# Performance work log

Hardware: AMD Instinct MI355X
Metric: run time of the kernel (lower is better)

Reference implementation:

```python
import jax, jax.numpy as jnp
import numpy as np

D_MODEL = 1024
NUM_HEAD = 16
D_K = D_MODEL // NUM_HEAD


def setup_inputs() -> dict:
    key = jax.random.key(0)
    ks = jax.random.split(key, 9)
    s = 1.0 / np.sqrt(D_MODEL)
    return {
        "x": jax.random.normal(ks[0], (2, 2048, D_MODEL), dtype=jnp.float32),
        "Wq": jax.random.normal(ks[1], (D_MODEL, D_MODEL), dtype=jnp.float32) * s,
        "bq": jax.random.normal(ks[2], (D_MODEL,), dtype=jnp.float32) * s,
        "Wk": jax.random.normal(ks[3], (D_MODEL, D_MODEL), dtype=jnp.float32) * s,
        "bk": jax.random.normal(ks[4], (D_MODEL,), dtype=jnp.float32) * s,
        "Wv": jax.random.normal(ks[5], (D_MODEL, D_MODEL), dtype=jnp.float32) * s,
        "bv": jax.random.normal(ks[6], (D_MODEL,), dtype=jnp.float32) * s,
        "Wo": jax.random.normal(ks[7], (D_MODEL, D_MODEL), dtype=jnp.float32) * s,
        "bo": jax.random.normal(ks[8], (D_MODEL,), dtype=jnp.float32) * s,
    }


def reference(x, Wq, bq, Wk, bk, Wv, bv, Wo, bo):
    B, S, _ = x.shape
    # QKV projections: [B,S,D] -> [B,H,S,d_k]
    def proj(W, b):
        y = jnp.einsum("bsd,df->bsf", x, W) + b
        return y.reshape(B, S, NUM_HEAD, D_K).transpose(0, 2, 1, 3)

    Q = proj(Wq, bq)
    K = proj(Wk, bk)
    V = proj(Wv, bv)
    scale = 1.0 / jnp.sqrt(jnp.asarray(D_K, dtype=x.dtype))
    attn = jnp.einsum("bhqd,bhkd->bhqk", Q, K) * scale  # [B,H,S,S]
    probs = jax.nn.softmax(attn, axis=-1)
    out = jnp.einsum("bhqk,bhkd->bhqd", probs, V)  # [B,H,S,d_k]
    out = out.transpose(0, 2, 1, 3).reshape(B, S, D_MODEL)
    return jnp.einsum("bsd,df->bsf", out, Wo) + bo
```

## Files before the change

### kernel.cpp

```cpp
#include <hip/hip_runtime.h>
#include <hip/hip_bf16.h>
#include <math.h>

constexpr int DM = 1024;
constexpr int NH = 16;
constexpr int DK = 64;
constexpr int SQ = 2048;
constexpr int BB = 2;
constexpr int MR = BB * SQ;

typedef short bf16x8 __attribute__((ext_vector_type(8)));
typedef float f32x4 __attribute__((ext_vector_type(4)));

__device__ inline unsigned short f2bf(float f) {
  unsigned u = __float_as_uint(f);
  unsigned r = (u + 0x7fffu + ((u >> 16) & 1u)) >> 16;
  return (unsigned short)r;
}

__device__ inline int fswz(int r) { return (r & 7) ^ ((r >> 3) & 7); }
__device__ inline int swz(int r, int c) {
  return r * 64 + ((((c >> 3) ^ fswz(r)) & 7) << 3) + (c & 7);
}

__global__ __launch_bounds__(256)
void cast_kernel(const float* __restrict__ in, unsigned short* __restrict__ out, int n8) {
  int i = blockIdx.x * 256 + threadIdx.x;
  if (i >= n8) return;
  float4 a = *(const float4*)&in[(size_t)i * 8];
  float4 b = *(const float4*)&in[(size_t)i * 8 + 4];
  ushort4 lo = {f2bf(a.x), f2bf(a.y), f2bf(a.z), f2bf(a.w)};
  ushort4 hi = {f2bf(b.x), f2bf(b.y), f2bf(b.z), f2bf(b.w)};
  *(ushort4*)&out[(size_t)i * 8] = lo;
  *(ushort4*)&out[(size_t)i * 8 + 4] = hi;
}

__global__ __launch_bounds__(256)
void transpose_cast_kernel(const float* __restrict__ W, unsigned short* __restrict__ Wt) {
  __shared__ float tl[32][33];
  const int tx = threadIdx.x & 31, ty = threadIdx.x >> 5;
  const int x0 = blockIdx.x * 32, y0 = blockIdx.y * 32;
  #pragma unroll
  for (int i = 0; i < 4; ++i)
    tl[ty + i * 8][tx] = W[(size_t)(y0 + ty + i * 8) * DM + x0 + tx];
  __syncthreads();
  #pragma unroll
  for (int i = 0; i < 4; ++i)
    Wt[(size_t)(x0 + ty + i * 8) * DM + y0 + tx] = f2bf(tl[tx][ty + i * 8]);
}

template<int MODE>
__global__ __launch_bounds__(256)
void mfma_gemm(const unsigned short* __restrict__ A, const unsigned short* __restrict__ Bt,
               const float* __restrict__ bias, void* __restrict__ outp)
{
  constexpr int K = DM, N = DM;
  __shared__ unsigned short As[2][128 * 64];
  __shared__ unsigned short Bs[2][128 * 64];
  const int t = threadIdx.x;
  const int w = t >> 6, ln = t & 63;
  const int wr = w >> 1, wc = w & 1;
  const int rb = blockIdx.y * 128, cb = blockIdx.x * 128;

  f32x4 acc[4][4] = {};

  auto stage = [&](int buf, int k0) {
    #pragma unroll
    for (int j = 0; j < 4; ++j) {
      const int rows8 = (w * 4 + j) * 8;
      const int r = rows8 + (ln >> 3);
      const int gc = (((ln & 7) ^ fswz(r)) & 7) * 8;
      __builtin_amdgcn_global_load_lds(
          (const __attribute__((address_space(1))) void*)&A[(size_t)(rb + r) * K + k0 + gc],
          (__attribute__((address_space(3))) void*)&As[buf][rows8 * 64], 16, 0, 0);
      __builtin_amdgcn_global_load_lds(
          (const __attribute__((address_space(1))) void*)&Bt[(size_t)(cb + r) * K + k0 + gc],
          (__attribute__((address_space(3))) void*)&Bs[buf][rows8 * 64], 16, 0, 0);
    }
  };

  stage(0, 0);
  asm volatile("s_waitcnt vmcnt(0)" ::: "memory");
  __builtin_amdgcn_s_barrier();

  for (int it = 0; it < K / 64; ++it) {
    const int buf = it & 1;
    if (it < K / 64 - 1) stage(buf ^ 1, (it + 1) * 64);
    const int rsel = ln & 15;
    #pragma unroll
    for (int kk = 0; kk < 2; ++kk) {
      const int ko = kk * 32 + (ln >> 4) * 8;
      bf16x8 af[4], bfr[4];
      #pragma unroll
      for (int m = 0; m < 4; ++m)
        af[m] = *(const bf16x8*)&As[buf][swz(wr * 64 + m * 16 + rsel, ko)];
      #pragma unroll
      for (int n = 0; n < 4; ++n)
        bfr[n] = *(const bf16x8*)&Bs[buf][swz(wc * 64 + n * 16 + rsel, ko)];
      #pragma unroll
      for (int m = 0; m < 4; ++m)
        #pragma unroll
        for (int n = 0; n < 4; ++n)
          acc[m][n] = __builtin_amdgcn_mfma_f32_16x16x32_bf16(af[m], bfr[n], acc[m][n], 0, 0, 0);
    }
    asm volatile("s_waitcnt vmcnt(0)" ::: "memory");
    __builtin_amdgcn_s_barrier();
  }

  const int cl = ln & 15, rg = (ln >> 4) * 4;
  #pragma unroll
  for (int m = 0; m < 4; ++m) {
    #pragma unroll
    for (int i = 0; i < 4; ++i) {
      const int r = rb + wr * 64 + m * 16 + rg + i;
      #pragma unroll
      for (int n = 0; n < 4; ++n) {
        const int c = cb + wc * 64 + n * 16 + cl;
        float v = acc[m][n][i] + bias[c];
        if (MODE == 3) v *= 0.125f;
        if (MODE == 0) {
          ((float*)outp)[(size_t)r * N + c] = v;
        } else {
          const int b = r >> 11, s = r & 2047;
          const int h = c >> 6, d = c & 63;
          ((unsigned short*)outp)[(((size_t)(b * NH + h)) * SQ + s) * DK + d] = f2bf(v);
        }
      }
    }
  }
}

__global__ __launch_bounds__(512, 4)
void attn_mfma(const unsigned short* __restrict__ Qp, const unsigned short* __restrict__ Kp,
               const unsigned short* __restrict__ Vp, unsigned short* __restrict__ ctx)
{
  __shared__ unsigned short Qs[128 * 64];
  __shared__ unsigned short Ks[64 * 64];
  __shared__ unsigned short Vt[64 * 64];
  __shared__ unsigned short Pl[8 * 16 * 64];
  const int t = threadIdx.x, w = t >> 6, ln = t & 63;
  const int bh = blockIdx.y, q0 = blockIdx.x * 128;
  const unsigned short* Qb = Qp + (size_t)bh * SQ * DK;
  const unsigned short* Kb = Kp + (size_t)bh * SQ * DK;
  const unsigned short* Vb = Vp + (size_t)bh * SQ * DK;

  #pragma unroll
  for (int i = 0; i < 2; ++i) {
    int g = t + i * 512, r = g >> 3, cg = g & 7;
    uint4 qv = *(const uint4*)&Qb[(size_t)(q0 + r) * DK + cg * 8];
    *(uint4*)&Qs[r * 64 + (((cg ^ fswz(r)) & 7) << 3)] = qv;
  }
  __syncthreads();
  const int rsel = ln & 15, ko = (ln >> 4) * 8;
  bf16x8 qf[2];
  #pragma unroll
  for (int kw = 0; kw < 2; ++kw)
    qf[kw] = *(const bf16x8*)&Qs[swz(w * 16 + rsel, ko + 32 * kw)];

  f32x4 acc2[4] = {};
  float m = -1e30f, l = 0.f;

  const int r0 = t >> 3, cg0 = t & 7;
  uint4 kg = *(const uint4*)&Kb[(size_t)r0 * DK + cg0 * 8];
  uint4 vg = *(const uint4*)&Vb[(size_t)r0 * DK + cg0 * 8];

  for (int c0 = 0; c0 < SQ; c0 += 64) {
    __syncthreads();
    *(uint4*)&Ks[r0 * 64 + (((cg0 ^ fswz(r0)) & 7) << 3)] = kg;
    {
      const unsigned short* vv = (const unsigned short*)&vg;
      const int d0 = cg0 * 8;
      #pragma unroll
      for (int e = 0; e < 8; ++e)
        Vt[swz(d0 + e, r0)] = vv[e];
    }
    __syncthreads();

    if (c0 + 64 < SQ) {
      kg = *(const uint4*)&Kb[(size_t)(c0 + 64 + r0) * DK + cg0 * 8];
      vg = *(const uint4*)&Vb[(size_t)(c0 + 64 + r0) * DK + cg0 * 8];
    }

    f32x4 s[4] = {};
    #pragma unroll
    for (int kw = 0; kw < 2; ++kw)
      #pragma unroll
      for (int fr = 0; fr < 4; ++fr) {
        bf16x8 kf = *(const bf16x8*)&Ks[swz(fr * 16 + rsel, ko + 32 * kw)];
        s[fr] = __builtin_amdgcn_mfma_f32_16x16x32_bf16(kf, qf[kw], s[fr], 0, 0, 0);
      }

    float t0 = fmaxf(fmaxf(s[0][0], s[0][1]), fmaxf(s[0][2], s[0][3]));
    float t1 = fmaxf(fmaxf(s[1][0], s[1][1]), fmaxf(s[1][2], s[1][3]));
    float t2 = fmaxf(fmaxf(s[2][0], s[2][1]), fmaxf(s[2][2], s[2][3]));
    float t3 = fmaxf(fmaxf(s[3][0], s[3][1]), fmaxf(s[3][2], s[3][3]));
    float tm = fmaxf(fmaxf(t0, t1), fmaxf(t2, t3));
    tm = fmaxf(tm, __shfl_xor(tm, 16));
    tm = fmaxf(tm, __shfl_xor(tm, 32));

    if (__any((tm - m) > 8.f)) {
      const float mnew = fmaxf(m, tm);
      const float corr = __expf(m - mnew);
      float ci[4];
      #pragma unroll
      for (int i = 0; i < 4; ++i) ci[i] = __shfl(corr, (ln >> 4) * 4 + i);
      #pragma unroll
      for (int n = 0; n < 4; ++n)
        #pragma unroll
        for (int i = 0; i < 4; ++i) acc2[n][i] *= ci[i];
      l *= corr;
      m = mnew;
    }

    float p[4][4];
    #pragma unroll
    for (int fr = 0; fr < 4; ++fr)
      #pragma unroll
      for (int i = 0; i < 4; ++i)
        p[fr][i] = __expf(s[fr][i] - m);
    float a0 = (p[0][0] + p[0][1]) + (p[0][2] + p[0][3]);
    float a1 = (p[1][0] + p[1][1]) + (p[1][2] + p[1][3]);
    float a2 = (p[2][0] + p[2][1]) + (p[2][2] + p[2][3]);
    float a3 = (p[3][0] + p[3][1]) + (p[3][2] + p[3][3]);
    float ps = (a0 + a1) + (a2 + a3);
    ps += __shfl_xor(ps, 16);
    ps += __shfl_xor(ps, 32);
    l += ps;

    #pragma unroll
    for (int fr = 0; fr < 4; ++fr) {
      unsigned r01, r23;
      asm("v_cvt_pk_bf16_f32 %0, %1, %2" : "=v"(r01) : "v"(p[fr][0]), "v"(p[fr][1]));
      asm("v_cvt_pk_bf16_f32 %0, %1, %2" : "=v"(r23) : "v"(p[fr][2]), "v"(p[fr][3]));
      uint2 pv = {r01, r23};
      const int kk0 = (ln >> 4) * 4 + fr * 16;
      *(uint2*)&Pl[w * 1024 + swz(rsel, kk0)] = pv;
    }

    #pragma unroll
    for (int kw = 0; kw < 2; ++kw) {
      bf16x8 pf = *(const bf16x8*)&Pl[w * 1024 + swz(rsel, ko + 32 * kw)];
      #pragma unroll
      for (int n = 0; n < 4; ++n) {
        bf16x8 vf = *(const bf16x8*)&Vt[swz(n * 16 + rsel, ko + 32 * kw)];
        acc2[n] = __builtin_amdgcn_mfma_f32_16x16x32_bf16(pf, vf, acc2[n], 0, 0, 0);
      }
    }
  }

  const float rl = 1.0f / l;
  float ri[4];
  #pragma unroll
  for (int i = 0; i < 4; ++i) ri[i] = __shfl(rl, (ln >> 4) * 4 + i);
  const int b = bh >> 4, h = bh & 15;
  #pragma unroll
  for (int n = 0; n < 4; ++n)
    #pragma unroll
    for (int i = 0; i < 4; ++i) {
      const int srow = q0 + w * 16 + (ln >> 4) * 4 + i;
      ctx[((size_t)(b * SQ + srow)) * DM + h * 64 + n * 16 + rsel] =
          f2bf(acc2[n][i] * ri[i]);
    }
}

extern "C" void kernel_launch(void* const* d_in, const int* in_sizes, int n_in,
                              void* d_out, int out_size, void* d_ws, size_t ws_size,
                              hipStream_t stream) {
  const float* x  = (const float*)d_in[0];
  const float* Wq = (const float*)d_in[1];
  const float* bq = (const float*)d_in[2];
  const float* Wk = (const float*)d_in[3];
  const float* bk = (const float*)d_in[4];
  const float* Wv = (const float*)d_in[5];
  const float* bv = (const float*)d_in[6];
  const float* Wo = (const float*)d_in[7];
  const float* bo = (const float*)d_in[8];
  float* out = (float*)d_out;

  unsigned short* xb   = (unsigned short*)d_ws;
  unsigned short* Wtq  = xb  + (size_t)MR * DM;
  unsigned short* Wtk  = Wtq + (size_t)DM * DM;
  unsigned short* Wtv  = Wtk + (size_t)DM * DM;
  unsigned short* Wto  = Wtv + (size_t)DM * DM;
  unsigned short* Qb   = Wto + (size_t)DM * DM;
  unsigned short* Kb   = Qb  + (size_t)MR * DM;
  unsigned short* Vb   = Kb  + (size_t)MR * DM;
  unsigned short* ctxb = Vb  + (size_t)MR * DM;

  cast_kernel<<<(MR * DM / 8 + 255) / 256, 256, 0, stream>>>(x, xb, MR * DM / 8);
  dim3 tg(DM / 32, DM / 32);
  transpose_cast_kernel<<<tg, 256, 0, stream>>>(Wq, Wtq);
  transpose_cast_kernel<<<tg, 256, 0, stream>>>(Wk, Wtk);
  transpose_cast_kernel<<<tg, 256, 0, stream>>>(Wv, Wtv);
  transpose_cast_kernel<<<tg, 256, 0, stream>>>(Wo, Wto);

  dim3 gg(DM / 128, MR / 128);
  mfma_gemm<3><<<gg, 256, 0, stream>>>(xb, Wtq, bq, Qb);
  mfma_gemm<1><<<gg, 256, 0, stream>>>(xb, Wtk, bk, Kb);
  mfma_gemm<1><<<gg, 256, 0, stream>>>(xb, Wtv, bv, Vb);

  attn_mfma<<<dim3(SQ / 128, BB * NH), 512, 0, stream>>>(Qb, Kb, Vb, ctxb);

  mfma_gemm<0><<<gg, 256, 0, stream>>>(ctxb, Wto, bo, out);
}
```

Measured before the change: 176.2 us.

## Fuse QKV projections into one GEMM and double-buffer K/V in attention

Concatenates the transposed Wq/Wk/Wv and the three biases so a single GEMM launch with three times the column blocks produces Q, K and V in head-major layout, with Q pre-scaled. This removes two launches and gives better CU occupancy. The attention kernel now double-buffers the K/V LDS tiles, writing the next tile after the PV MFMAs, which needs one barrier per iteration instead of two. It also raises wave priority around the MFMA sections. LDS use in attention grows by 16KB, which could affect occupancy.

```diff
diff --git a/kernel.cpp b/kernel.cpp
--- a/kernel.cpp
+++ b/kernel.cpp
@@ -49,10 +49,96 @@
     Wt[(size_t)(x0 + ty + i * 8) * DM + y0 + tx] = f2bf(tl[tx][ty + i * 8]);
 }
 
-template<int MODE>
-__global__ __launch_bounds__(256)
-void mfma_gemm(const unsigned short* __restrict__ A, const unsigned short* __restrict__ Bt,
-               const float* __restrict__ bias, void* __restrict__ outp)
+__global__ __launch_bounds__(256)
+void concat_bias(const float* __restrict__ bq, const float* __restrict__ bk,
+                 const float* __restrict__ bv, float* __restrict__ cb) {
+  int i = blockIdx.x * 256 + threadIdx.x;
+  if (i < 1024) cb[i] = bq[i];
+  else if (i < 2048) cb[i] = bk[i - 1024];
+  else if (i < 3072) cb[i] = bv[i - 2048];
+}
+
+__global__ __launch_bounds__(256)
+void qkv_gemm(const unsigned short* __restrict__ A, const unsigned short* __restrict__ Wt3,
+              const float* __restrict__ cbias, unsigned short* __restrict__ qkv)
+{
+  constexpr int K = DM;
+  __shared__ unsigned short As[2][128 * 64];
+  __shared__ unsigned short Bs[2][128 * 64];
+  const int t = threadIdx.x;
+  const int w = t >> 6, ln = t & 63;
+  const int wr = w >> 1, wc = w & 1;
+  const int rb = blockIdx.y * 128, cb = blockIdx.x * 128;
+
+  f32x4 acc[4][4] = {};
+
+  auto stage = [&](int buf, int k0) {
+    #pragma unroll
+    for (int j = 0; j < 4; ++j) {
+      const int rows8 = (w * 4 + j) * 8;
+      const int r = rows8 + (ln >> 3);
+      const int gc = (((ln & 7) ^ fswz(r)) & 7) * 8;
+      __builtin_amdgcn_global_load_lds(
+          (const __attribute__((address_space(1))) void*)&A[(size_t)(rb + r) * K + k0 + gc],
+          (__attribute__((address_space(3))) void*)&As[buf][rows8 * 64], 16, 0, 0);
+      __builtin_amdgcn_global_load_lds(
+          (const __attribute__((address_space(1))) void*)&Wt3[(size_t)(cb + r) * K + k0 + gc],
+          (__attribute__((address_space(3))) void*)&Bs[buf][rows8 * 64], 16, 0, 0);
+    }
+  };
+
+  stage(0, 0);
+  asm volatile("s_waitcnt vmcnt(0)" ::: "memory");
+  __builtin_amdgcn_s_barrier();
+
+  for (int it = 0; it < K / 64; ++it) {
+    const int buf = it & 1;
+    if (it < K / 64 - 1) stage(buf ^ 1, (it + 1) * 64);
+    const int rsel = ln & 15;
+    #pragma unroll
+    for (int kk = 0; kk < 2; ++kk) {
+      const int ko = kk * 32 + (ln >> 4) * 8;
+      bf16x8 af[4], bfr[4];
+      #pragma unroll
+      for (int m = 0; m < 4; ++m)
+        af[m] = *(const bf16x8*)&As[buf][swz(wr * 64 + m * 16 + rsel, ko)];
+      #pragma unroll
+      for (int n = 0; n < 4; ++n)
+        bfr[n] = *(const bf16x8*)&Bs[buf][swz(wc * 64 + n * 16 + rsel, ko)];
+      #pragma unroll
+      for (int m = 0; m < 4; ++m)
+        #pragma unroll
+        for (int n = 0; n < 4; ++n)
+          acc[m][n] = __builtin_amdgcn_mfma_f32_16x16x32_bf16(af[m], bfr[n], acc[m][n], 0, 0, 0);
+    }
+    asm volatile("s_waitcnt vmcnt(0)" ::: "memory");
+    __builtin_amdgcn_s_barrier();
+  }
+
+  const int cl = ln & 15, rg = (ln >> 4) * 4;
+  const int which = cb >> 10;
+  const float sc = (which == 0) ? 0.125f : 1.0f;
+  unsigned short* dst0 = qkv + (size_t)which * MR * DM;
+  #pragma unroll
+  for (int m = 0; m < 4; ++m) {
+    #pragma unroll
+    for (int i = 0; i < 4; ++i) {
+      const int r = rb + wr * 64 + m * 16 + rg + i;
+      const int b = r >> 11, s = r & 2047;
+      #pragma unroll
+      for (int n = 0; n < 4; ++n) {
+        const int c = cb + wc * 64 + n * 16 + cl;
+        const float v = (acc[m][n][i] + cbias[c]) * sc;
+        const int cc = c & 1023, h = cc >> 6, d = c & 63;
+        dst0[(((size_t)(b * NH + h)) * SQ + s) * DK + d] = f2bf(v);
+      }
+    }
+  }
+}
+
+__global__ __launch_bounds__(256)
+void mfma_gemm_out(const unsigned short* __restrict__ A, const unsigned short* __restrict__ Bt,
+                   const float* __restrict__ bias, float* __restrict__ outp)
 {
   constexpr int K = DM, N = DM;
   __shared__ unsigned short As[2][128 * 64];
@@ -116,15 +202,7 @@
       #pragma unroll
       for (int n = 0; n < 4; ++n) {
         const int c = cb + wc * 64 + n * 16 + cl;
-        float v = acc[m][n][i] + bias[c];
-        if (MODE == 3) v *= 0.125f;
-        if (MODE == 0) {
-          ((float*)outp)[(size_t)r * N + c] = v;
-        } else {
-          const int b = r >> 11, s = r & 2047;
-          const int h = c >> 6, d = c & 63;
-          ((unsigned short*)outp)[(((size_t)(b * NH + h)) * SQ + s) * DK + d] = f2bf(v);
-        }
+        outp[(size_t)r * N + c] = acc[m][n][i] + bias[c];
       }
     }
   }
@@ -135,8 +213,8 @@
                const unsigned short* __restrict__ Vp, unsigned short* __restrict__ ctx)
 {
   __shared__ unsigned short Qs[128 * 64];
-  __shared__ unsigned short Ks[64 * 64];
-  __shared__ unsigned short Vt[64 * 64];
+  __shared__ unsigned short Ks[2][64 * 64];
+  __shared__ unsigned short Vt[2][64 * 64];
   __shared__ unsigned short Pl[8 * 16 * 64];
   const int t = threadIdx.x, w = t >> 6, ln = t & 63;
   const int bh = blockIdx.y, q0 = blockIdx.x * 128;
@@ -161,34 +239,37 @@
   float m = -1e30f, l = 0.f;
 
   const int r0 = t >> 3, cg0 = t & 7;
-  uint4 kg = *(const uint4*)&Kb[(size_t)r0 * DK + cg0 * 8];
-  uint4 vg = *(const uint4*)&Vb[(size_t)r0 * DK + cg0 * 8];
-
+  const int ksl = r0 * 64 + (((cg0 ^ fswz(r0)) & 7) << 3);
+  {
+    uint4 kg = *(const uint4*)&Kb[(size_t)r0 * DK + cg0 * 8];
+    uint4 vg = *(const uint4*)&Vb[(size_t)r0 * DK + cg0 * 8];
+    *(uint4*)&Ks[0][ksl] = kg;
+    const unsigned short* vv = (const unsigned short*)&vg;
+    #pragma unroll
+    for (int e = 0; e < 8; ++e)
+      Vt[0][swz(cg0 * 8 + e, r0)] = vv[e];
+  }
+  __syncthreads();
+
+  int cur = 0;
   for (int c0 = 0; c0 < SQ; c0 += 64) {
-    __syncthreads();
-    *(uint4*)&Ks[r0 * 64 + (((cg0 ^ fswz(r0)) & 7) << 3)] = kg;
-    {
-      const unsigned short* vv = (const unsigned short*)&vg;
-      const int d0 = cg0 * 8;
-      #pragma unroll
-      for (int e = 0; e < 8; ++e)
-        Vt[swz(d0 + e, r0)] = vv[e];
-    }
-    __syncthreads();
-
-    if (c0 + 64 < SQ) {
+    const bool haveNext = (c0 + 64 < SQ);
+    uint4 kg, vg;
+    if (haveNext) {
       kg = *(const uint4*)&Kb[(size_t)(c0 + 64 + r0) * DK + cg0 * 8];
       vg = *(const uint4*)&Vb[(size_t)(c0 + 64 + r0) * DK + cg0 * 8];
     }
 
     f32x4 s[4] = {};
+    __builtin_amdgcn_s_setprio(1);
     #pragma unroll
     for (int kw = 0; kw < 2; ++kw)
       #pragma unroll
       for (int fr = 0; fr < 4; ++fr) {
-        bf16x8 kf = *(const bf16x8*)&Ks[swz(fr * 16 + rsel, ko + 32 * kw)];
+        bf16x8 kf = *(const bf16x8*)&Ks[cur][swz(fr * 16 + rsel, ko + 32 * kw)];
         s[fr] = __builtin_amdgcn_mfma_f32_16x16x32_bf16(kf, qf[kw], s[fr], 0, 0, 0);
       }
+    __builtin_amdgcn_s_setprio(0);
 
     float t0 = fmaxf(fmaxf(s[0][0], s[0][1]), fmaxf(s[0][2], s[0][3]));
     float t1 = fmaxf(fmaxf(s[1][0], s[1][1]), fmaxf(s[1][2], s[1][3]));
@@ -237,15 +318,27 @@
       *(uint2*)&Pl[w * 1024 + swz(rsel, kk0)] = pv;
     }
 
+    __builtin_amdgcn_s_setprio(1);
     #pragma unroll
     for (int kw = 0; kw < 2; ++kw) {
       bf16x8 pf = *(const bf16x8*)&Pl[w * 1024 + swz(rsel, ko + 32 * kw)];
       #pragma unroll
       for (int n = 0; n < 4; ++n) {
-        bf16x8 vf = *(const bf16x8*)&Vt[swz(n * 16 + rsel, ko + 32 * kw)];
+        bf16x8 vf = *(const bf16x8*)&Vt[cur][swz(n * 16 + rsel, ko + 32 * kw)];
         acc2[n] = __builtin_amdgcn_mfma_f32_16x16x32_bf16(pf, vf, acc2[n], 0, 0, 0);
       }
     }
+    __builtin_amdgcn_s_setprio(0);
+
+    if (haveNext) {
+      *(uint4*)&Ks[cur ^ 1][ksl] = kg;
+      const unsigned short* vv = (const unsigned short*)&vg;
+      #pragma unroll
+      for (int e = 0; e < 8; ++e)
+        Vt[cur ^ 1][swz(cg0 * 8 + e, r0)] = vv[e];
+      __syncthreads();
+    }
+    cur ^= 1;
   }
 
   const float rl = 1.0f / l;
@@ -277,29 +370,25 @@
   const float* bo = (const float*)d_in[8];
   float* out = (float*)d_out;
 
-  unsigned short* xb   = (unsigned short*)d_ws;
-  unsigned short* Wtq  = xb  + (size_t)MR * DM;
-  unsigned short* Wtk  = Wtq + (size_t)DM * DM;
-  unsigned short* Wtv  = Wtk + (size_t)DM * DM;
-  unsigned short* Wto  = Wtv + (size_t)DM * DM;
-  unsigned short* Qb   = Wto + (size_t)DM * DM;
-  unsigned short* Kb   = Qb  + (size_t)MR * DM;
-  unsigned short* Vb   = Kb  + (size_t)MR * DM;
-  unsigned short* ctxb = Vb  + (size_t)MR * DM;
+  unsigned short* xb    = (unsigned short*)d_ws;
+  unsigned short* Wt3   = xb   + (size_t)MR * DM;
+  unsigned short* Wto   = Wt3  + (size_t)3 * DM * DM;
+  unsigned short* QKVb  = Wto  + (size_t)DM * DM;
+  unsigned short* ctxb  = QKVb + (size_t)3 * MR * DM;
+  float*          cbias = (float*)(ctxb + (size_t)MR * DM);
 
   cast_kernel<<<(MR * DM / 8 + 255) / 256, 256, 0, stream>>>(x, xb, MR * DM / 8);
   dim3 tg(DM / 32, DM / 32);
-  transpose_cast_kernel<<<tg, 256, 0, stream>>>(Wq, Wtq);
-  transpose_cast_kernel<<<tg, 256, 0, stream>>>(Wk, Wtk);
-  transpose_cast_kernel<<<tg, 256, 0, stream>>>(Wv, Wtv);
+  transpose_cast_kernel<<<tg, 256, 0, stream>>>(Wq, Wt3);
+  transpose_cast_kernel<<<tg, 256, 0, stream>>>(Wk, Wt3 + (size_t)DM * DM);
+  transpose_cast_kernel<<<tg, 256, 0, stream>>>(Wv, Wt3 + (size_t)2 * DM * DM);
   transpose_cast_kernel<<<tg, 256, 0, stream>>>(Wo, Wto);
-
-  dim3 gg(DM / 128, MR / 128);
-  mfma_gemm<3><<<gg, 256, 0, stream>>>(xb, Wtq, bq, Qb);
-  mfma_gemm<1><<<gg, 256, 0, stream>>>(xb, Wtk, bk, Kb);
-  mfma_gemm<1><<<gg, 256, 0, stream>>>(xb, Wtv, bv, Vb);
-
-  attn_mfma<<<dim3(SQ / 128, BB * NH), 512, 0, stream>>>(Qb, Kb, Vb, ctxb);
-
-  mfma_gemm<0><<<gg, 256, 0, stream>>>(ctxb, Wto, bo, out);
-}
+  concat_bias<<<12, 256, 0, stream>>>(bq, bk, bv, cbias);
+
+  qkv_gemm<<<dim3(3 * DM / 128, MR / 128), 256, 0, stream>>>(xb, Wt3, cbias, QKVb);
+
+  attn_mfma<<<dim3(SQ / 128, BB * NH), 512, 0, stream>>>(
+      QKVb, QKVb + (size_t)MR * DM, QKVb + (size_t)2 * MR * DM, ctxb);
+
+  mfma_gemm_out<<<dim3(DM / 128, MR / 128), 256, 0, stream>>>(ctxb, Wto, bo, out);
+}
```

New measurement: 155.7 us. 11.7% less time.
